# Kernel optimization log

Hardware: AMD Instinct MI355X
Metric: run time of the kernel (lower is better)

Reference implementation:

```python
import jax, jax.numpy as jnp
import numpy as np
from jax import lax

B, N, K = 8, 4096, 64
RATIO1, R1 = 0.5, 0.2
RATIO2, R2 = 0.25, 0.4
SA1_DIMS = [3, 32, 32, 64]
SA2_DIMS = [64 + 3, 64, 64, 128]
SA3_DIMS = [128 + 3, 128, 256, 512]


def _mlp_params(key, dims, prefix):
    params = {}
    for i, (din, dout) in enumerate(zip(dims[:-1], dims[1:])):
        key, k1 = jax.random.split(key)
        s = 1.0 / np.sqrt(din)
        params[f"{prefix}_w{i}"] = jax.random.uniform(k1, (din, dout), jnp.float32, -s, s)
        params[f"{prefix}_b{i}"] = jnp.zeros((dout,), jnp.float32)
    return params, key


def setup_inputs() -> dict:
    key = jax.random.key(0)
    key, kp = jax.random.split(key)
    inp = {"pos": jax.random.uniform(kp, (B, N, 3), jnp.float32)}  # unit-cube point clouds
    p1, key = _mlp_params(key, SA1_DIMS, "sa1"); inp.update(p1)
    p2, key = _mlp_params(key, SA2_DIMS, "sa2"); inp.update(p2)
    p3, key = _mlp_params(key, SA3_DIMS, "sa3"); inp.update(p3)
    key, k1, k2 = jax.random.split(key, 3)
    s = 1.0 / np.sqrt(512)
    inp["w_mu"] = jax.random.uniform(k1, (512, 32), jnp.float32, -s, s)
    inp["b_mu"] = jnp.zeros((32,), jnp.float32)
    inp["w_lv"] = jax.random.uniform(k2, (512, 32), jnp.float32, -s, s)
    inp["b_lv"] = jnp.zeros((32,), jnp.float32)
    return inp


def _mlp(x, params):
    # PyG MLP semantics (plain_last=True): ReLU on all but the final layer.
    for i, (w, b) in enumerate(params):
        x = x @ w + b
        if i < len(params) - 1:
            x = jax.nn.relu(x)
    return x


def _fps(pos, M):
    # Farthest point sampling, deterministic start at index 0. pos: [N,3] -> [M]
    n = pos.shape[0]
    def step(carry, _):
        dist, far = carry
        d = jnp.sum((pos - pos[far]) ** 2, axis=-1)
        dist = jnp.minimum(dist, d)
        return (dist, jnp.argmax(dist).astype(jnp.int32)), far
    _, idx = lax.scan(step, (jnp.full(n, jnp.inf, pos.dtype), jnp.int32(0)), None, length=M)
    return idx


def _sa(x, pos, ratio, r, params):
    # SAModule: FPS -> radius query (K nearest within r) -> gather -> MLP -> masked max
    Nn = pos.shape[1]
    M = int(round(ratio * Nn))
    idx = jax.vmap(lambda p: _fps(p, M))(pos)                 # [B,M]
    centers = jax.vmap(lambda p, i: p[i])(pos, idx)           # [B,M,3]
    d2 = jnp.sum((centers[:, :, None, :] - pos[:, None, :, :]) ** 2, axis=-1)  # [B,M,N]
    neg = jnp.where(d2 <= r * r, -d2, -jnp.inf)
    vals, nbr = lax.top_k(neg, K)                             # [B,M,K]
    mask = vals > -jnp.inf                                    # valid neighbors (self always valid)
    pos_j = jax.vmap(lambda p, i: p[i])(pos, nbr)             # [B,M,K,3]
    rel = pos_j - centers[:, :, None, :]
    if x is None:
        feat = rel
    else:
        x_j = jax.vmap(lambda f, i: f[i])(x, nbr)             # [B,M,K,C]
        feat = jnp.concatenate([x_j, rel], axis=-1)
    h = _mlp(feat, params)                                    # [B,M,K,C']
    h = jnp.where(mask[..., None], h, -jnp.inf)
    out = jnp.max(h, axis=2)                                  # scatter-max aggregation
    out = jnp.where(jnp.isfinite(out), out, 0.0)
    return out, centers


def reference(pos, sa1_w0, sa1_b0, sa1_w1, sa1_b1, sa1_w2, sa1_b2,
              sa2_w0, sa2_b0, sa2_w1, sa2_b1, sa2_w2, sa2_b2,
              sa3_w0, sa3_b0, sa3_w1, sa3_b1, sa3_w2, sa3_b2,
              w_mu, b_mu, w_lv, b_lv):
    p1 = [(sa1_w0, sa1_b0), (sa1_w1, sa1_b1), (sa1_w2, sa1_b2)]
    p2 = [(sa2_w0, sa2_b0), (sa2_w1, sa2_b1), (sa2_w2, sa2_b2)]
    p3 = [(sa3_w0, sa3_b0), (sa3_w1, sa3_b1), (sa3_w2, sa3_b2)]
    x1, pos1 = _sa(None, pos, RATIO1, R1, p1)                 # [B,2048,64]
    x2, pos2 = _sa(x1, pos1, RATIO2, R2, p2)                  # [B,512,128]
    g = _mlp(jnp.concatenate([x2, pos2], axis=-1), p3)        # [B,512,512]
    feat = jnp.max(g, axis=1)                                 # global max pool [B,512]
    mu = feat @ w_mu + b_mu
    log_var = feat @ w_lv + b_lv
    eps = jax.random.normal(jax.random.key(42), mu.shape, mu.dtype)
    z = mu + eps * jnp.exp(0.5 * log_var)
    return (z, mu, log_var)
```

## Files before the change

kernel.cpp:

```cpp
#include <hip/hip_runtime.h>
#include <cstdint>
#include <cstddef>


constexpr int BATCH = 8;
constexpr int NPT0  = 4096;
constexpr int M1    = 2048;
constexpr int M2    = 512;
constexpr int KNB   = 64;
constexpr int CAP   = 1024;

constexpr size_t O_WT1S1 = 0;
constexpr size_t O_WT2S1 = 96;
constexpr size_t O_WT3S1 = 1120;
constexpr size_t O_WT1S2 = 3168;
constexpr size_t O_WT2S2 = 7456;
constexpr size_t O_WT3S2 = 11552;
constexpr size_t O_WT1S3 = 19744;
constexpr size_t O_WT2S3 = 36512;
constexpr size_t O_POS1  = 69280;
constexpr size_t O_X1    = 118432;
constexpr size_t O_POS2  = 1167008;
constexpr size_t O_X2    = 1179296;
constexpr size_t O_H2G   = O_X1;
constexpr size_t O_FP    = O_X2;

template <int C>
__device__ __forceinline__ int dppmov(int x) {
  return __builtin_amdgcn_update_dpp(x, x, C, 0xF, 0xF, false);
}

__device__ __forceinline__ float wave_fmax_scal(float x) {
  x = fmaxf(x, __int_as_float(dppmov<0x111>(__float_as_int(x))));
  x = fmaxf(x, __int_as_float(dppmov<0x112>(__float_as_int(x))));
  x = fmaxf(x, __int_as_float(dppmov<0x114>(__float_as_int(x))));
  x = fmaxf(x, __int_as_float(dppmov<0x118>(__float_as_int(x))));
  x = fmaxf(x, __int_as_float(dppmov<0x142>(__float_as_int(x))));
  x = fmaxf(x, __int_as_float(dppmov<0x143>(__float_as_int(x))));
  return __int_as_float(__builtin_amdgcn_readlane(__float_as_int(x), 63));
}

template <int C>
__device__ __forceinline__ void dpp_key_max(uint32_t& lo, uint32_t& hi) {
  uint32_t olo = (uint32_t)dppmov<C>((int)lo);
  uint32_t ohi = (uint32_t)dppmov<C>((int)hi);
  bool bet = (ohi > hi) || (ohi == hi && olo > lo);
  lo = bet ? olo : lo;
  hi = bet ? ohi : hi;
}
__device__ __forceinline__ void wave_key_max_scal(uint32_t& lo, uint32_t& hi) {
  dpp_key_max<0x111>(lo, hi);
  dpp_key_max<0x112>(lo, hi);
  dpp_key_max<0x114>(lo, hi);
  dpp_key_max<0x118>(lo, hi);
  dpp_key_max<0x142>(lo, hi);
  dpp_key_max<0x143>(lo, hi);
  lo = (uint32_t)__builtin_amdgcn_readlane((int)lo, 63);
  hi = (uint32_t)__builtin_amdgcn_readlane((int)hi, 63);
}
template <int C>
__device__ __forceinline__ void dpp_key_min(uint32_t& lo, uint32_t& hi) {
  uint32_t olo = (uint32_t)dppmov<C>((int)lo);
  uint32_t ohi = (uint32_t)dppmov<C>((int)hi);
  bool bet = (ohi < hi) || (ohi == hi && olo < lo);
  lo = bet ? olo : lo;
  hi = bet ? ohi : hi;
}
__device__ __forceinline__ void wave_key_min_scal(uint32_t& lo, uint32_t& hi) {
  dpp_key_min<0x111>(lo, hi);
  dpp_key_min<0x112>(lo, hi);
  dpp_key_min<0x114>(lo, hi);
  dpp_key_min<0x118>(lo, hi);
  dpp_key_min<0x142>(lo, hi);
  dpp_key_min<0x143>(lo, hi);
  lo = (uint32_t)__builtin_amdgcn_readlane((int)lo, 63);
  hi = (uint32_t)__builtin_amdgcn_readlane((int)hi, 63);
}

__device__ __forceinline__ uint32_t rotl32(uint32_t x, int d) {
  return (x << d) | (x >> (32 - d));
}

__device__ __forceinline__ void threefry_0_42(uint32_t c0, uint32_t c1,
                                              uint32_t& o0, uint32_t& o1) {
  const uint32_t k0 = 0u, k1 = 42u;
  const uint32_t ks[3] = {k0, k1, k0 ^ k1 ^ 0x1BD11BDAu};
  uint32_t x0 = c0 + ks[0];
  uint32_t x1 = c1 + ks[1];
  const int R0[4] = {13, 15, 26, 6};
  const int R1[4] = {17, 29, 16, 24};
  #pragma unroll
  for (int g = 0; g < 5; ++g) {
    const int* R = (g & 1) ? R1 : R0;
    #pragma unroll
    for (int r = 0; r < 4; ++r) {
      x0 += x1;
      x1 = rotl32(x1, R[r]);
      x1 ^= x0;
    }
    x0 += ks[(g + 1) % 3];
    x1 += ks[(g + 2) % 3] + (uint32_t)(g + 1);
  }
  o0 = x0; o1 = x1;
}

__device__ __forceinline__ float erfinv_xla(float x) {
  float w = -log1pf(-x * x);
  float p;
  if (w < 5.0f) {
    w = w - 2.5f;
    p = 2.81022636e-08f;
    p = fmaf(p, w, 3.43273939e-07f);
    p = fmaf(p, w, -3.5233877e-06f);
    p = fmaf(p, w, -4.39150654e-06f);
    p = fmaf(p, w, 0.00021858087f);
    p = fmaf(p, w, -0.00125372503f);
    p = fmaf(p, w, -0.00417768164f);
    p = fmaf(p, w, 0.246640727f);
    p = fmaf(p, w, 1.50140941f);
  } else {
    w = sqrtf(w) - 3.0f;
    p = -0.000200214257f;
    p = fmaf(p, w, 0.000100950558f);
    p = fmaf(p, w, 0.00134934322f);
    p = fmaf(p, w, -0.00367342844f);
    p = fmaf(p, w, 0.00573950773f);
    p = fmaf(p, w, -0.0076224613f);
    p = fmaf(p, w, 0.00943887047f);
    p = fmaf(p, w, 1.00167406f);
    p = fmaf(p, w, 2.83297682f);
  }
  return p * x;
}

__global__ __launch_bounds__(256) void prep_transpose(
    const float* __restrict__ a0, const float* __restrict__ a1,
    const float* __restrict__ a2, const float* __restrict__ a3,
    const float* __restrict__ a4, const float* __restrict__ a5,
    const float* __restrict__ a6, const float* __restrict__ a7,
    float* __restrict__ ws) {
  int u = blockIdx.x * 256 + threadIdx.x;
  if (u < 96)    { ws[O_WT1S1 + u] = a0[(u % 3)   * 32  + u / 3];   return; } u -= 96;
  if (u < 1024)  { ws[O_WT2S1 + u] = a1[(u % 32)  * 32  + u / 32];  return; } u -= 1024;
  if (u < 2048)  { ws[O_WT3S1 + u] = a2[(u % 32)  * 64  + u / 32];  return; } u -= 2048;
  if (u < 4288)  { ws[O_WT1S2 + u] = a3[(u % 67)  * 64  + u / 67];  return; } u -= 4288;
  if (u < 4096)  { ws[O_WT2S2 + u] = a4[(u % 64)  * 64  + u / 64];  return; } u -= 4096;
  if (u < 8192)  { ws[O_WT3S2 + u] = a5[(u % 64)  * 128 + u / 64];  return; } u -= 8192;
  if (u < 16768) { ws[O_WT1S3 + u] = a6[(u % 131) * 128 + u / 131]; return; } u -= 16768;
  if (u < 32768) { ws[O_WT2S3 + u] = a7[(u % 128) * 256 + u / 128]; return; }
}

template <int N, int M, int T>
__global__ __launch_bounds__(T) void fps_kernel(const float* __restrict__ pos,
                                                float* __restrict__ centers) {
  constexpr int PPT = N / T;
  constexpr int NW  = T / 64;
  __shared__ float4 ps[N];
  __shared__ float4 candA[2][NW];
  __shared__ float  candZ[2][NW];
  const int tid  = threadIdx.x;
  const int lane = tid & 63;
  const int wid  = tid >> 6;
  const int b    = blockIdx.x;
  const float* pb = pos + (size_t)b * N * 3;

  float mx[PPT], my[PPT], mz[PPT], md[PPT];
  #pragma unroll
  for (int s = 0; s < PPT; ++s) {
    int i = s * T + tid;
    float x = pb[i * 3 + 0], y = pb[i * 3 + 1], z = pb[i * 3 + 2];
    ps[i] = make_float4(x, y, z, 0.0f);
    mx[s] = x; my[s] = y; mz[s] = z;
    md[s] = __builtin_inff();
  }
  __syncthreads();

  float4 c0 = ps[0];
  float cx = c0.x, cy = c0.y, cz = c0.z;
  float* cb = centers + (size_t)b * M * 3;

  for (int m = 0; m < M; ++m) {
    if (tid == 0) { cb[m * 3 + 0] = cx; cb[m * 3 + 1] = cy; cb[m * 3 + 2] = cz; }
    float bv = -1.0f;
    int   bi = 0x7FFFFFFF;
    {
      #pragma clang fp contract(off)
      #pragma unroll
      for (int s = 0; s < PPT; ++s) {
        float dx = mx[s] - cx, dy = my[s] - cy, dz = mz[s] - cz;
        float d = (dx * dx + dy * dy) + dz * dz;
        float nd = fminf(md[s], d);
        md[s] = nd;
        if (nd > bv) { bv = nd; bi = s * T + tid; }
      }
    }
    uint32_t klo = ~(uint32_t)bi;
    uint32_t khi = __float_as_uint(bv);
    wave_key_max_scal(klo, khi);
    int p = (int)~klo;

    float4 cw = ps[p];
    if (lane == 0) {
      candA[m & 1][wid] = make_float4(__uint_as_float(khi),
                                      __uint_as_float(klo), cw.x, cw.y);
      candZ[m & 1][wid] = cw.z;
    }
    __syncthreads();
    float4 aw0 = candA[m & 1][0];
    uint32_t Khi = __float_as_uint(aw0.x), Klo = __float_as_uint(aw0.y);
    float wx = aw0.z, wy = aw0.w, wz = candZ[m & 1][0];
    #pragma unroll
    for (int w = 1; w < NW; ++w) {
      float4 aw = candA[m & 1][w];
      float zz = candZ[m & 1][w];
      uint32_t ohi = __float_as_uint(aw.x), olo = __float_as_uint(aw.y);
      bool bet = (ohi > Khi) || (ohi == Khi && olo > Klo);
      Khi = bet ? ohi : Khi;
      Klo = bet ? olo : Klo;
      wx  = bet ? aw.z : wx;
      wy  = bet ? aw.w : wy;
      wz  = bet ? zz   : wz;
    }
    cx = wx; cy = wy; cz = wz;
  }
}

template <int NPTS, int DF, int D1, int D2, int DOUT>
__global__ __launch_bounds__(64) void sa_kernel(
    const float* __restrict__ pts, const float* __restrict__ feats,
    const float* __restrict__ centers, float* __restrict__ outf,
    const float* __restrict__ wt1, const float* __restrict__ bz1,
    const float* __restrict__ wt2, const float* __restrict__ bz2,
    const float* __restrict__ wt3, const float* __restrict__ bz3,
    int M, float r2max) {
  constexpr int DIN = DF + 3;
  constexpr int S1  = D1 + 4;
  constexpr int S2  = D2 + 4;
  __shared__ float sd[CAP];
  __shared__ int   si[CAP];
  __shared__ float hb1[64 * S1];
  __shared__ float hb2[64 * S2];

  const int lane = threadIdx.x;
  const int bm = blockIdx.x;
  const int b = bm / M, m = bm % M;
  const float* pb = pts + (size_t)b * NPTS * 3;
  const float* cc = centers + ((size_t)b * M + m) * 3;
  const float cx = cc[0], cy = cc[1], cz = cc[2];

  int cnt = 0;
  const unsigned long long ltmask = (1ull << lane) - 1ull;
  for (int base = 0; base < NPTS; base += 64) {
    int i = base + lane;
    float x3 = pb[i * 3 + 0], y3 = pb[i * 3 + 1], z3 = pb[i * 3 + 2];
    float d2;
    {
      #pragma clang fp contract(off)
      float dx = cx - x3, dy = cy - y3, dz = cz - z3;
      d2 = (dx * dx + dy * dy) + dz * dz;
    }
    bool inr = (d2 <= r2max);
    unsigned long long mk = __ballot(inr);
    int p = cnt + (int)__popcll(mk & ltmask);
    if (inr && p < CAP) { sd[p] = d2; si[p] = i; }
    cnt += (int)__popcll(mk);
  }
  if (cnt > CAP) cnt = CAP;
  __syncthreads();

  int my_nbr = -1;
  if (cnt <= KNB) {
    my_nbr = (lane < cnt) ? si[lane] : -1;
  } else {
    constexpr int SMAX = CAP / 64;
    float rd[SMAX];
    #pragma unroll
    for (int s = 0; s < SMAX; ++s) {
      rd[s] = __builtin_inff();
      if (s * 64 < cnt) {
        int q = s * 64 + lane;
        if (q < cnt) rd[s] = sd[q];
      }
    }
    for (int k = 0; k < KNB; ++k) {
      float bv = rd[0];
      int   bp = lane;
      #pragma unroll
      for (int s = 1; s < SMAX; ++s) {
        if (s * 64 < cnt) {
          if (rd[s] < bv) { bv = rd[s]; bp = s * 64 + lane; }
        }
      }
      uint32_t klo = (uint32_t)bp;
      uint32_t khi = __float_as_uint(bv);
      wave_key_min_scal(klo, khi);
      int bpw = (int)klo;
      if (lane == k) my_nbr = si[bpw];
      int wl = bpw & 63, wsl = bpw >> 6;
      #pragma unroll
      for (int s = 0; s < SMAX; ++s) {
        if (s * 64 < cnt) {
          rd[s] = (lane == wl && s == wsl) ? __builtin_inff() : rd[s];
        }
      }
    }
  }
  const bool valid = (my_nbr >= 0);
  const int safeN = valid ? my_nbr : 0;

  float rel[3];
  {
    const float* pr = pb + (size_t)safeN * 3;
    rel[0] = pr[0] - cx; rel[1] = pr[1] - cy; rel[2] = pr[2] - cz;
  }
  float xin[DF > 0 ? DF : 1];
  if constexpr (DF > 0) {
    const float* xr = feats + ((size_t)b * NPTS + safeN) * DF;
    #pragma unroll
    for (int i = 0; i < DF; i += 4) {
      float4 v = *reinterpret_cast<const float4*>(xr + i);
      xin[i] = v.x; xin[i + 1] = v.y; xin[i + 2] = v.z; xin[i + 3] = v.w;
    }
  }

  float* r1 = hb1 + lane * S1;
  for (int c = 0; c < D1; c += 4) {
    const float* w0 = wt1 + (c + 0) * DIN;
    const float* w1 = wt1 + (c + 1) * DIN;
    const float* w2 = wt1 + (c + 2) * DIN;
    const float* w3 = wt1 + (c + 3) * DIN;
    float a0 = bz1[c + 0], a1 = bz1[c + 1], a2 = bz1[c + 2], a3 = bz1[c + 3];
    if constexpr (DF > 0) {
      #pragma unroll
      for (int i = 0; i < DF; ++i) {
        a0 = fmaf(xin[i], w0[i], a0);
        a1 = fmaf(xin[i], w1[i], a1);
        a2 = fmaf(xin[i], w2[i], a2);
        a3 = fmaf(xin[i], w3[i], a3);
      }
    }
    #pragma unroll
    for (int r = 0; r < 3; ++r) {
      a0 = fmaf(rel[r], w0[DF + r], a0);
      a1 = fmaf(rel[r], w1[DF + r], a1);
      a2 = fmaf(rel[r], w2[DF + r], a2);
      a3 = fmaf(rel[r], w3[DF + r], a3);
    }
    *reinterpret_cast<float4*>(r1 + c) =
        make_float4(fmaxf(a0, 0.0f), fmaxf(a1, 0.0f),
                    fmaxf(a2, 0.0f), fmaxf(a3, 0.0f));
  }
  float h1[D1];
  #pragma unroll
  for (int i = 0; i < D1; i += 4) {
    float4 v = *reinterpret_cast<const float4*>(r1 + i);
    h1[i] = v.x; h1[i + 1] = v.y; h1[i + 2] = v.z; h1[i + 3] = v.w;
  }

  float* rr2 = hb2 + lane * S2;
  for (int c = 0; c < D2; c += 4) {
    const float* w0 = wt2 + (c + 0) * D1;
    const float* w1 = wt2 + (c + 1) * D1;
    const float* w2 = wt2 + (c + 2) * D1;
    const float* w3 = wt2 + (c + 3) * D1;
    float a0 = bz2[c + 0], a1 = bz2[c + 1], a2 = bz2[c + 2], a3 = bz2[c + 3];
    #pragma unroll
    for (int i = 0; i < D1; ++i) {
      a0 = fmaf(h1[i], w0[i], a0);
      a1 = fmaf(h1[i], w1[i], a1);
      a2 = fmaf(h1[i], w2[i], a2);
      a3 = fmaf(h1[i], w3[i], a3);
    }
    *reinterpret_cast<float4*>(rr2 + c) =
        make_float4(fmaxf(a0, 0.0f), fmaxf(a1, 0.0f),
                    fmaxf(a2, 0.0f), fmaxf(a3, 0.0f));
  }
  float h2[D2];
  #pragma unroll
  for (int i = 0; i < D2; i += 4) {
    float4 v = *reinterpret_cast<const float4*>(rr2 + i);
    h2[i] = v.x; h2[i + 1] = v.y; h2[i + 2] = v.z; h2[i + 3] = v.w;
  }

  float* orow = outf + ((size_t)b * M + m) * DOUT;
  #pragma unroll
  for (int u = 0; u < DOUT / 64; ++u) {
    float outv = 0.0f;
    for (int ccb = 0; ccb < 64; ccb += 4) {
      const int c = u * 64 + ccb;
      const float* w0 = wt3 + (c + 0) * D2;
      const float* w1 = wt3 + (c + 1) * D2;
      const float* w2 = wt3 + (c + 2) * D2;
      const float* w3 = wt3 + (c + 3) * D2;
      float a0 = bz3[c + 0], a1 = bz3[c + 1], a2 = bz3[c + 2], a3 = bz3[c + 3];
      #pragma unroll
      for (int i = 0; i < D2; ++i) {
        a0 = fmaf(h2[i], w0[i], a0);
        a1 = fmaf(h2[i], w1[i], a1);
        a2 = fmaf(h2[i], w2[i], a2);
        a3 = fmaf(h2[i], w3[i], a3);
      }
      const float NI = -__builtin_inff();
      float s0 = wave_fmax_scal(valid ? a0 : NI);
      float s1 = wave_fmax_scal(valid ? a1 : NI);
      float s2 = wave_fmax_scal(valid ? a2 : NI);
      float s3 = wave_fmax_scal(valid ? a3 : NI);
      if (lane == ccb + 0) outv = s0;
      if (lane == ccb + 1) outv = s1;
      if (lane == ccb + 2) outv = s2;
      if (lane == ccb + 3) outv = s3;
    }
    orow[u * 64 + lane] = outv;
  }
}

__global__ __launch_bounds__(256) void sa3_l12_kernel(
    const float* __restrict__ x2, const float* __restrict__ pos2,
    const float* __restrict__ wt1, const float* __restrict__ bz1,
    const float* __restrict__ wt2, const float* __restrict__ bz2,
    float* __restrict__ h2g) {
  __shared__ float H[64 * 132];
  const int tid = threadIdx.x;
  const int lane = tid & 63, w = tid >> 6;
  const int b = blockIdx.x >> 3, tile = blockIdx.x & 7;
  const int pt = tile * 64 + lane;
  const float* xrow = x2 + ((size_t)b * 512 + pt) * 128;
  float* hrow = H + lane * 132;
  const int c0 = w * 32;

  float f[64];
  #pragma unroll
  for (int i = 0; i < 64; i += 4) {
    float4 v = *reinterpret_cast<const float4*>(xrow + i);
    f[i] = v.x; f[i + 1] = v.y; f[i + 2] = v.z; f[i + 3] = v.w;
  }
  for (int c = c0; c < c0 + 32; ++c) {
    const float* wv = wt1 + c * 131;
    float acc = bz1[c];
    #pragma unroll
    for (int i = 0; i < 64; ++i) acc = fmaf(f[i], wv[i], acc);
    hrow[c] = acc;
  }
  #pragma unroll
  for (int i = 0; i < 64; i += 4) {
    float4 v = *reinterpret_cast<const float4*>(xrow + 64 + i);
    f[i] = v.x; f[i + 1] = v.y; f[i + 2] = v.z; f[i + 3] = v.w;
  }
  float q0, q1, q2;
  {
    const float* pr = pos2 + ((size_t)b * 512 + pt) * 3;
    q0 = pr[0]; q1 = pr[1]; q2 = pr[2];
  }
  for (int c = c0; c < c0 + 32; ++c) {
    const float* wv = wt1 + c * 131 + 64;
    float acc = hrow[c];
    #pragma unroll
    for (int i = 0; i < 64; ++i) acc = fmaf(f[i], wv[i], acc);
    acc = fmaf(q0, wv[64], acc);
    acc = fmaf(q1, wv[65], acc);
    acc = fmaf(q2, wv[66], acc);
    hrow[c] = fmaxf(acc, 0.0f);
  }
  __syncthreads();

  float h[128];
  #pragma unroll
  for (int i = 0; i < 128; i += 4) {
    float4 v = *reinterpret_cast<const float4*>(hrow + i);
    h[i] = v.x; h[i + 1] = v.y; h[i + 2] = v.z; h[i + 3] = v.w;
  }
  float* grow = h2g + ((size_t)b * 512 + pt) * 256;
  const int c1 = w * 64;
  for (int c = c1; c < c1 + 64; ++c) {
    const float* wv = wt2 + c * 128;
    float acc = bz2[c];
    #pragma unroll
    for (int i = 0; i < 128; ++i) acc = fmaf(h[i], wv[i], acc);
    grow[c] = fmaxf(acc, 0.0f);
  }
}

__global__ __launch_bounds__(256) void sa3_l3_kernel(
    const float* __restrict__ h2g, const float* __restrict__ w3,
    const float* __restrict__ bz3, float* __restrict__ fpart) {
  const int tid = threadIdx.x;
  const int blk = blockIdx.x;
  const int b   = blk >> 6;
  const int t16 = (blk >> 1) & 31;
  const int cb  = blk & 1;
  const int c = cb * 256 + tid;
  const float* hbase = h2g + ((size_t)b * 512 + t16 * 16) * 256;

  float acc[16];
  #pragma unroll
  for (int j = 0; j < 16; ++j) acc[j] = 0.0f;

  for (int i0 = 0; i0 < 256; i0 += 8) {
    float wv[8];
    #pragma unroll
    for (int u = 0; u < 8; ++u) wv[u] = w3[(size_t)(i0 + u) * 512 + c];
    #pragma unroll
    for (int j = 0; j < 16; ++j) {
      const float* hr = hbase + (size_t)j * 256 + i0;
      #pragma unroll
      for (int u = 0; u < 8; ++u) acc[j] = fmaf(hr[u], wv[u], acc[j]);
    }
  }
  float mv = acc[0];
  #pragma unroll
  for (int j = 1; j < 16; ++j) mv = fmaxf(mv, acc[j]);
  fpart[((size_t)b * 32 + t16) * 512 + c] = mv + bz3[c];
}

__global__ __launch_bounds__(64) void final_kernel(
    const float* __restrict__ fpart,
    const float* __restrict__ wmu, const float* __restrict__ bmu,
    const float* __restrict__ wlv, const float* __restrict__ blv,
    float* __restrict__ outp) {
  __shared__ float feat[512];
  const int tid = threadIdx.x;
  const int b = blockIdx.x;
  for (int cidx = tid; cidx < 512; cidx += 64) {
    float mv = fpart[(size_t)b * 32 * 512 + cidx];
    #pragma unroll
    for (int t = 1; t < 32; ++t)
      mv = fmaxf(mv, fpart[((size_t)b * 32 + t) * 512 + cidx]);
    feat[cidx] = mv;
  }
  __syncthreads();
  if (tid < 32) {
    const int c = tid;
    double amu = 0.0, alv = 0.0;
    for (int i = 0; i < 512; ++i) {
      double fv = (double)feat[i];
      amu += fv * (double)wmu[i * 32 + c];
      alv += fv * (double)wlv[i * 32 + c];
    }
    float mu = (float)amu + bmu[c];
    float lv = (float)alv + blv[c];

    uint32_t n = (uint32_t)(b * 32 + c);
    uint32_t o0, o1;
    threefry_0_42(0u, n, o0, o1);
    uint32_t bits = o0 ^ o1;
    float fl = __uint_as_float((bits >> 9) | 0x3f800000u) - 1.0f;
    const float LO = -0.99999994039535522461f;
    float u = fl * 2.0f + LO;
    u = fmaxf(LO, u);
    float eps = 1.4142135623730951f * erfinv_xla(u);
    float z = mu + eps * expf(0.5f * lv);

    outp[b * 32 + c] = z;
    outp[256 + b * 32 + c] = mu;
    outp[512 + b * 32 + c] = lv;
  }
}

extern "C" void kernel_launch(void* const* d_in, const int* in_sizes, int n_in,
                              void* d_out, int out_size, void* d_ws, size_t ws_size,
                              hipStream_t stream) {
  (void)in_sizes; (void)n_in; (void)out_size; (void)ws_size;
  const float* pos  = (const float*)d_in[0];
  const float* s1w0 = (const float*)d_in[1];  const float* s1b0 = (const float*)d_in[2];
  const float* s1w1 = (const float*)d_in[3];  const float* s1b1 = (const float*)d_in[4];
  const float* s1w2 = (const float*)d_in[5];  const float* s1b2 = (const float*)d_in[6];
  const float* s2w0 = (const float*)d_in[7];  const float* s2b0 = (const float*)d_in[8];
  const float* s2w1 = (const float*)d_in[9];  const float* s2b1 = (const float*)d_in[10];
  const float* s2w2 = (const float*)d_in[11]; const float* s2b2 = (const float*)d_in[12];
  const float* s3w0 = (const float*)d_in[13]; const float* s3b0 = (const float*)d_in[14];
  const float* s3w1 = (const float*)d_in[15]; const float* s3b1 = (const float*)d_in[16];
  const float* s3w2 = (const float*)d_in[17]; const float* s3b2 = (const float*)d_in[18];
  const float* wmu  = (const float*)d_in[19]; const float* bmu  = (const float*)d_in[20];
  const float* wlv  = (const float*)d_in[21]; const float* blv  = (const float*)d_in[22];
  float* ws = (float*)d_ws;
  float* out = (float*)d_out;

  prep_transpose<<<271, 256, 0, stream>>>(s1w0, s1w1, s1w2, s2w0, s2w1, s2w2,
                                          s3w0, s3w1, ws);

  fps_kernel<NPT0, M1, 512><<<BATCH, 512, 0, stream>>>(pos, ws + O_POS1);

  sa_kernel<NPT0, 0, 32, 32, 64><<<BATCH * M1, 64, 0, stream>>>(
      pos, nullptr, ws + O_POS1, ws + O_X1,
      ws + O_WT1S1, s1b0, ws + O_WT2S1, s1b1, ws + O_WT3S1, s1b2,
      M1, 0.04f);

  fps_kernel<M1, M2, 512><<<BATCH, 512, 0, stream>>>(ws + O_POS1, ws + O_POS2);

  sa_kernel<M1, 64, 64, 64, 128><<<BATCH * M2, 64, 0, stream>>>(
      ws + O_POS1, ws + O_X1, ws + O_POS2, ws + O_X2,
      ws + O_WT1S2, s2b0, ws + O_WT2S2, s2b1, ws + O_WT3S2, s2b2,
      M2, 0.16f);

  sa3_l12_kernel<<<BATCH * 8, 256, 0, stream>>>(
      ws + O_X2, ws + O_POS2, ws + O_WT1S3, s3b0, ws + O_WT2S3, s3b1,
      ws + O_H2G);

  sa3_l3_kernel<<<BATCH * 64, 256, 0, stream>>>(ws + O_H2G, s3w2, s3b2,
                                                ws + O_FP);

  final_kernel<<<BATCH, 64, 0, stream>>>(ws + O_FP, wmu, bmu, wlv, blv, out);
}
```

Measured before the change: 4.119 ms.

## Overlap FPS with SA grouping via progress flags in fused persistent kernels

Fuses each FPS kernel with its following SA kernel into one launch. Eight blocks run FPS at raised priority and publish progress every 64 centers through an atomic counter. The remaining blocks each pack 8 waves, and each wave spins on that counter until its center is ready, so the MLP/grouping work overlaps the serial FPS loop instead of waiting for it to finish. It also drops the LDS staging of hidden activations in favour of registers and replaces a block barrier with a wave-local LDS wait. The risks are spin-wait overhead, a deadlock if the FPS blocks are not scheduled before the waiting blocks fill the GPU, and higher register pressure.

```diff
diff --git a/kernel.cpp b/kernel.cpp
--- a/kernel.cpp
+++ b/kernel.cpp
@@ -24,6 +24,7 @@
 constexpr size_t O_X2    = 1179296;
 constexpr size_t O_H2G   = O_X1;
 constexpr size_t O_FP    = O_X2;
+constexpr size_t O_PROG  = 1703584;
 
 template <int C>
 __device__ __forceinline__ int dppmov(int x) {
@@ -75,6 +76,10 @@
   dpp_key_min<0x143>(lo, hi);
   lo = (uint32_t)__builtin_amdgcn_readlane((int)lo, 63);
   hi = (uint32_t)__builtin_amdgcn_readlane((int)hi, 63);
+}
+
+__device__ __forceinline__ void wave_lds_fence() {
+  asm volatile("s_waitcnt lgkmcnt(0)" ::: "memory");
 }
 
 __device__ __forceinline__ uint32_t rotl32(uint32_t x, int d) {
@@ -139,7 +144,9 @@
     const float* __restrict__ a4, const float* __restrict__ a5,
     const float* __restrict__ a6, const float* __restrict__ a7,
     float* __restrict__ ws) {
-  int u = blockIdx.x * 256 + threadIdx.x;
+  int u0 = blockIdx.x * 256 + threadIdx.x;
+  if (u0 < 16) ((int*)(ws + O_PROG))[u0] = 0;
+  int u = u0;
   if (u < 96)    { ws[O_WT1S1 + u] = a0[(u % 3)   * 32  + u / 3];   return; } u -= 96;
   if (u < 1024)  { ws[O_WT2S1 + u] = a1[(u % 32)  * 32  + u / 32];  return; } u -= 1024;
   if (u < 2048)  { ws[O_WT3S1 + u] = a2[(u % 32)  * 64  + u / 32];  return; } u -= 2048;
@@ -151,17 +158,20 @@
 }
 
 template <int N, int M, int T>
-__global__ __launch_bounds__(T) void fps_kernel(const float* __restrict__ pos,
-                                                float* __restrict__ centers) {
+__device__ __forceinline__ void fps_body(const float* __restrict__ pos,
+                                         float* __restrict__ centers,
+                                         int* __restrict__ prog,
+                                         char* smem, int b) {
   constexpr int PPT = N / T;
   constexpr int NW  = T / 64;
-  __shared__ float4 ps[N];
-  __shared__ float4 candA[2][NW];
-  __shared__ float  candZ[2][NW];
+  float* px = (float*)smem;
+  float* py = px + N;
+  float* pz = py + N;
+  float4* candA = (float4*)(pz + N);
+  float*  candZ = (float*)(candA + 2 * NW);
   const int tid  = threadIdx.x;
   const int lane = tid & 63;
   const int wid  = tid >> 6;
-  const int b    = blockIdx.x;
   const float* pb = pos + (size_t)b * N * 3;
 
   float mx[PPT], my[PPT], mz[PPT], md[PPT];
@@ -169,18 +179,22 @@
   for (int s = 0; s < PPT; ++s) {
     int i = s * T + tid;
     float x = pb[i * 3 + 0], y = pb[i * 3 + 1], z = pb[i * 3 + 2];
-    ps[i] = make_float4(x, y, z, 0.0f);
+    px[i] = x; py[i] = y; pz[i] = z;
     mx[s] = x; my[s] = y; mz[s] = z;
     md[s] = __builtin_inff();
   }
   __syncthreads();
 
-  float4 c0 = ps[0];
-  float cx = c0.x, cy = c0.y, cz = c0.z;
+  float cx = px[0], cy = py[0], cz = pz[0];
   float* cb = centers + (size_t)b * M * 3;
 
   for (int m = 0; m < M; ++m) {
-    if (tid == 0) { cb[m * 3 + 0] = cx; cb[m * 3 + 1] = cy; cb[m * 3 + 2] = cz; }
+    if (tid == 0) {
+      cb[m * 3 + 0] = cx; cb[m * 3 + 1] = cy; cb[m * 3 + 2] = cz;
+      if ((m & 63) == 63)
+        __hip_atomic_store(prog + b, m + 1, __ATOMIC_RELEASE,
+                           __HIP_MEMORY_SCOPE_AGENT);
+    }
     float bv = -1.0f;
     int   bi = 0x7FFFFFFF;
     {
@@ -199,53 +213,61 @@
     wave_key_max_scal(klo, khi);
     int p = (int)~klo;
 
-    float4 cw = ps[p];
+    float wx = px[p], wy = py[p], wz = pz[p];
     if (lane == 0) {
-      candA[m & 1][wid] = make_float4(__uint_as_float(khi),
-                                      __uint_as_float(klo), cw.x, cw.y);
-      candZ[m & 1][wid] = cw.z;
+      candA[(m & 1) * NW + wid] =
+          make_float4(__uint_as_float(khi), __uint_as_float(klo), wx, wy);
+      candZ[(m & 1) * NW + wid] = wz;
     }
     __syncthreads();
-    float4 aw0 = candA[m & 1][0];
+    float4 aw0 = candA[(m & 1) * NW + 0];
     uint32_t Khi = __float_as_uint(aw0.x), Klo = __float_as_uint(aw0.y);
-    float wx = aw0.z, wy = aw0.w, wz = candZ[m & 1][0];
+    float sx = aw0.z, sy = aw0.w, sz = candZ[(m & 1) * NW + 0];
     #pragma unroll
     for (int w = 1; w < NW; ++w) {
-      float4 aw = candA[m & 1][w];
-      float zz = candZ[m & 1][w];
+      float4 aw = candA[(m & 1) * NW + w];
+      float zz = candZ[(m & 1) * NW + w];
       uint32_t ohi = __float_as_uint(aw.x), olo = __float_as_uint(aw.y);
       bool bet = (ohi > Khi) || (ohi == Khi && olo > Klo);
       Khi = bet ? ohi : Khi;
       Klo = bet ? olo : Klo;
-      wx  = bet ? aw.z : wx;
-      wy  = bet ? aw.w : wy;
-      wz  = bet ? zz   : wz;
-    }
-    cx = wx; cy = wy; cz = wz;
-  }
-}
-
-template <int NPTS, int DF, int D1, int D2, int DOUT>
-__global__ __launch_bounds__(64) void sa_kernel(
+      sx  = bet ? aw.z : sx;
+      sy  = bet ? aw.w : sy;
+      sz  = bet ? zz   : sz;
+    }
+    cx = sx; cy = sy; cz = sz;
+  }
+}
+
+template <int NPTS, int DF, int D1, int D2, int DOUT, int MM>
+__device__ __forceinline__ void sa_body(
     const float* __restrict__ pts, const float* __restrict__ feats,
     const float* __restrict__ centers, float* __restrict__ outf,
     const float* __restrict__ wt1, const float* __restrict__ bz1,
     const float* __restrict__ wt2, const float* __restrict__ bz2,
     const float* __restrict__ wt3, const float* __restrict__ bz3,
-    int M, float r2max) {
+    float r2max, int* __restrict__ prog, char* smem) {
   constexpr int DIN = DF + 3;
-  constexpr int S1  = D1 + 4;
-  constexpr int S2  = D2 + 4;
-  __shared__ float sd[CAP];
-  __shared__ int   si[CAP];
-  __shared__ float hb1[64 * S1];
-  __shared__ float hb2[64 * S2];
-
-  const int lane = threadIdx.x;
-  const int bm = blockIdx.x;
-  const int b = bm / M, m = bm % M;
+  const int lane = threadIdx.x & 63;
+  const int wid  = threadIdx.x >> 6;
+  const int g = ((int)blockIdx.x - 8) * 8 + wid;
+  const int b = g / MM, m = g % MM;
+  float* sd = (float*)(smem + wid * 8192);
+  int*   si = (int*)(smem + wid * 8192 + 4096);
+
+  for (;;) {
+    int r = 0;
+    if (lane == 0)
+      r = __hip_atomic_load(prog + b, __ATOMIC_ACQUIRE,
+                            __HIP_MEMORY_SCOPE_AGENT);
+    r = __builtin_amdgcn_readfirstlane(r);
+    if (r > m) break;
+    __builtin_amdgcn_s_sleep(2);
+  }
+  __builtin_amdgcn_fence(__ATOMIC_ACQUIRE, "agent");
+
   const float* pb = pts + (size_t)b * NPTS * 3;
-  const float* cc = centers + ((size_t)b * M + m) * 3;
+  const float* cc = centers + ((size_t)b * MM + m) * 3;
   const float cx = cc[0], cy = cc[1], cz = cc[2];
 
   int cnt = 0;
@@ -266,7 +288,7 @@
     cnt += (int)__popcll(mk);
   }
   if (cnt > CAP) cnt = CAP;
-  __syncthreads();
+  wave_lds_fence();
 
   int my_nbr = -1;
   if (cnt <= KNB) {
@@ -323,7 +345,7 @@
     }
   }
 
-  float* r1 = hb1 + lane * S1;
+  float h1[D1];
   for (int c = 0; c < D1; c += 4) {
     const float* w0 = wt1 + (c + 0) * DIN;
     const float* w1 = wt1 + (c + 1) * DIN;
@@ -346,18 +368,13 @@
       a2 = fmaf(rel[r], w2[DF + r], a2);
       a3 = fmaf(rel[r], w3[DF + r], a3);
     }
-    *reinterpret_cast<float4*>(r1 + c) =
-        make_float4(fmaxf(a0, 0.0f), fmaxf(a1, 0.0f),
-                    fmaxf(a2, 0.0f), fmaxf(a3, 0.0f));
-  }
-  float h1[D1];
-  #pragma unroll
-  for (int i = 0; i < D1; i += 4) {
-    float4 v = *reinterpret_cast<const float4*>(r1 + i);
-    h1[i] = v.x; h1[i + 1] = v.y; h1[i + 2] = v.z; h1[i + 3] = v.w;
-  }
-
-  float* rr2 = hb2 + lane * S2;
+    h1[c + 0] = fmaxf(a0, 0.0f);
+    h1[c + 1] = fmaxf(a1, 0.0f);
+    h1[c + 2] = fmaxf(a2, 0.0f);
+    h1[c + 3] = fmaxf(a3, 0.0f);
+  }
+
+  float h2[D2];
   for (int c = 0; c < D2; c += 4) {
     const float* w0 = wt2 + (c + 0) * D1;
     const float* w1 = wt2 + (c + 1) * D1;
@@ -371,18 +388,13 @@
       a2 = fmaf(h1[i], w2[i], a2);
       a3 = fmaf(h1[i], w3[i], a3);
     }
-    *reinterpret_cast<float4*>(rr2 + c) =
-        make_float4(fmaxf(a0, 0.0f), fmaxf(a1, 0.0f),
-                    fmaxf(a2, 0.0f), fmaxf(a3, 0.0f));
-  }
-  float h2[D2];
-  #pragma unroll
-  for (int i = 0; i < D2; i += 4) {
-    float4 v = *reinterpret_cast<const float4*>(rr2 + i);
-    h2[i] = v.x; h2[i + 1] = v.y; h2[i + 2] = v.z; h2[i + 3] = v.w;
-  }
-
-  float* orow = outf + ((size_t)b * M + m) * DOUT;
+    h2[c + 0] = fmaxf(a0, 0.0f);
+    h2[c + 1] = fmaxf(a1, 0.0f);
+    h2[c + 2] = fmaxf(a2, 0.0f);
+    h2[c + 3] = fmaxf(a3, 0.0f);
+  }
+
+  float* orow = outf + ((size_t)b * MM + m) * DOUT;
   #pragma unroll
   for (int u = 0; u < DOUT / 64; ++u) {
     float outv = 0.0f;
@@ -414,6 +426,40 @@
   }
 }
 
+__global__ __launch_bounds__(512, 2) void stageA_kernel(
+    const float* __restrict__ pos, float* __restrict__ ws,
+    const float* __restrict__ bz1, const float* __restrict__ bz2,
+    const float* __restrict__ bz3) {
+  extern __shared__ char smem[];
+  int* prog = (int*)(ws + O_PROG);
+  if (blockIdx.x < 8) {
+    asm volatile("s_setprio 3");
+    fps_body<NPT0, M1, 512>(pos, ws + O_POS1, prog, smem, blockIdx.x);
+  } else {
+    sa_body<NPT0, 0, 32, 32, 64, M1>(
+        pos, nullptr, ws + O_POS1, ws + O_X1,
+        ws + O_WT1S1, bz1, ws + O_WT2S1, bz2, ws + O_WT3S1, bz3,
+        0.04f, prog, smem);
+  }
+}
+
+__global__ __launch_bounds__(512, 2) void stageB_kernel(
+    float* __restrict__ ws,
+    const float* __restrict__ bz1, const float* __restrict__ bz2,
+    const float* __restrict__ bz3) {
+  extern __shared__ char smem[];
+  int* prog = (int*)(ws + O_PROG) + 8;
+  if (blockIdx.x < 8) {
+    asm volatile("s_setprio 3");
+    fps_body<M1, M2, 512>(ws + O_POS1, ws + O_POS2, prog, smem, blockIdx.x);
+  } else {
+    sa_body<M1, 64, 64, 64, 128, M2>(
+        ws + O_POS1, ws + O_X1, ws + O_POS2, ws + O_X2,
+        ws + O_WT1S2, bz1, ws + O_WT2S2, bz2, ws + O_WT3S2, bz3,
+        0.16f, prog, smem);
+  }
+}
+
 __global__ __launch_bounds__(256) void sa3_l12_kernel(
     const float* __restrict__ x2, const float* __restrict__ pos2,
     const float* __restrict__ wt1, const float* __restrict__ bz1,
@@ -578,19 +624,11 @@
   prep_transpose<<<271, 256, 0, stream>>>(s1w0, s1w1, s1w2, s2w0, s2w1, s2w2,
                                           s3w0, s3w1, ws);
 
-  fps_kernel<NPT0, M1, 512><<<BATCH, 512, 0, stream>>>(pos, ws + O_POS1);
-
-  sa_kernel<NPT0, 0, 32, 32, 64><<<BATCH * M1, 64, 0, stream>>>(
-      pos, nullptr, ws + O_POS1, ws + O_X1,
-      ws + O_WT1S1, s1b0, ws + O_WT2S1, s1b1, ws + O_WT3S1, s1b2,
-      M1, 0.04f);
-
-  fps_kernel<M1, M2, 512><<<BATCH, 512, 0, stream>>>(ws + O_POS1, ws + O_POS2);
-
-  sa_kernel<M1, 64, 64, 64, 128><<<BATCH * M2, 64, 0, stream>>>(
-      ws + O_POS1, ws + O_X1, ws + O_POS2, ws + O_X2,
-      ws + O_WT1S2, s2b0, ws + O_WT2S2, s2b1, ws + O_WT3S2, s2b2,
-      M2, 0.16f);
+  stageA_kernel<<<8 + (BATCH * M1) / 8, 512, 65536, stream>>>(
+      pos, ws, s1b0, s1b1, s1b2);
+
+  stageB_kernel<<<8 + (BATCH * M2) / 8, 512, 65536, stream>>>(
+      ws, s2b0, s2b1, s2b2);
 
   sa3_l12_kernel<<<BATCH * 8, 256, 0, stream>>>(
       ws + O_X2, ws + O_POS2, ws + O_WT1S3, s3b0, ws + O_WT2S3, s3b1,
```

Result: faster. 3.887 ms (-5.6%).
